# Kernel tuning notes

Measured on AMD Instinct MI355X. Metric: run time of the kernel, lower is better.

Reference implementation:

```python
import jax, jax.numpy as jnp
import numpy as np

B, F, E = 16384, 50, 64          # batch, field_size, embedding_size
V, D = 100000, 512               # feature_size, deep_init_size
H1, H2 = 1024, 512               # deep_layers
BN_EPS = 1e-10


def setup_inputs() -> dict:
    key = jax.random.key(0)
    ks = jax.random.split(key, 14)
    g0 = np.sqrt(6.0 / (D + H1))
    g1 = np.sqrt(6.0 / (H1 + H2))
    go = np.sqrt(5.0 / (D + 1))
    return {
        "feat_index": jax.random.randint(ks[0], (B, F), 0, V),
        "feat_value": jax.random.uniform(ks[1], (B, F), dtype=jnp.float32),
        "feature_embeddings": jax.random.normal(ks[2], (V, E), dtype=jnp.float32) * 0.01,
        "product_linear": jax.random.normal(ks[3], (D, F, E), dtype=jnp.float32) * 0.01,
        "product_bias": jax.random.normal(ks[4], (D,), dtype=jnp.float32),
        "product_quadratic_inner": jax.random.normal(ks[5], (D, F), dtype=jnp.float32) * 0.01,
        "layer_0": jax.random.uniform(ks[6], (D, H1), minval=-g0, maxval=g0, dtype=jnp.float32),
        "bias_0": jax.random.uniform(ks[7], (1, H1), minval=-g0, maxval=g0, dtype=jnp.float32),
        "layer_1": jax.random.uniform(ks[8], (H1, H2), minval=-g1, maxval=g1, dtype=jnp.float32),
        "bias_1": jax.random.uniform(ks[9], (1, H2), minval=-g1, maxval=g1, dtype=jnp.float32),
        "bn_scale": jax.random.normal(ks[10], (1,), dtype=jnp.float32) * 0.01,
        "bn_offset": jax.random.normal(ks[11], (1,), dtype=jnp.float32) * 0.01,
        "output_w": jax.random.uniform(ks[12], (H2, 1), minval=-go, maxval=go, dtype=jnp.float32),
        "output_b": jnp.float32(0.01),
    }


def reference(feat_index, feat_value, feature_embeddings, product_linear,
              product_bias, product_quadratic_inner, layer_0, bias_0,
              layer_1, bias_1, bn_scale, bn_offset, output_w, output_b):
    # embedding lookup scaled by feature values: (B, F, E)
    emb = feature_embeddings[feat_index] * feat_value[..., None]
    # linear product signal: sum over field+embed dims for each of D units
    lz = jnp.einsum('bfe,dfe->bd', emb, product_linear)          # (B, D)
    # inner quadratic signal: field-weighted sum then L2 norm over embed dim
    s = jnp.einsum('bfe,df->bde', emb, product_quadratic_inner)  # (B, D, E)
    lp = jnp.sqrt(jnp.sum(s * s, axis=-1))                       # (B, D)
    y = jax.nn.relu(lz + lp + product_bias)
    # dropout omitted (deterministic eval-mode reference)
    for W, bvec in ((layer_0, bias_0), (layer_1, bias_1)):
        y = y @ W + bvec
        m = jnp.mean(y, axis=0)
        v = jnp.var(y, axis=0)
        y = (y - m) * jax.lax.rsqrt(v + BN_EPS) * bn_scale + bn_offset
        y = jax.nn.relu(y)
    out = y @ output_w + output_b
    return jax.nn.sigmoid(out)
```

## Files before the change

### kernel.cpp

```cpp
#include <hip/hip_runtime.h>

typedef unsigned short u16;
typedef __attribute__((ext_vector_type(8))) short bf16x8v;
typedef __attribute__((ext_vector_type(4))) float f32x4v;

#define B_SZ 16384
#define F_SZ 50
#define E_SZ 64
#define D_SZ 512
#define H1_SZ 1024
#define H2_SZ 512
#define KP 4096

__device__ __forceinline__ float b2f(u16 u){
  union { unsigned int i; float f; } v; v.i = ((unsigned int)u) << 16; return v.f;
}
__device__ __forceinline__ u16 f2b(float f){
  union { float f; unsigned int i; } v; v.f = f;
  unsigned int r = v.i + 0x7FFFu + ((v.i >> 16) & 1u);
  return (u16)(r >> 16);
}

__device__ __forceinline__ void gload16(const u16* g, u16* lds_base_uniform){
#if __has_builtin(__builtin_amdgcn_global_load_lds)
  __builtin_amdgcn_global_load_lds(
      (const __attribute__((address_space(1))) unsigned int*)g,
      (__attribute__((address_space(3))) unsigned int*)lds_base_uniform,
      16, 0, 0);
#else
  int lane = threadIdx.x & 63;
  *(uint4*)(lds_base_uniform + lane*8) = *(const uint4*)g;
#endif
}

__device__ __forceinline__ void swz(int id, int nblog2, int &x, int &y){
  int xcd = id & 7, j = id >> 3;
  x = j & ((1 << nblog2) - 1);
  y = ((j >> nblog2) << 3) | xcd;
}

__global__ __launch_bounds__(256) void k_gather(
    const int* __restrict__ fidx, const float* __restrict__ fval,
    const float* __restrict__ femb, u16* __restrict__ embT)
{
  __shared__ int   sidx[F_SZ];
  __shared__ float sfv[F_SZ];
  __shared__ u16   tile[F_SZ*66];
  const int b = blockIdx.x, t = threadIdx.x;
  if (t < F_SZ){ sidx[t] = fidx[b*F_SZ+t]; sfv[t] = fval[b*F_SZ+t]; }
  __syncthreads();
  #pragma unroll
  for (int i=0;i<13;i++){
    int k = i*256+t;
    if (k < F_SZ*E_SZ){
      int f = k>>6, e = k&63;
      tile[f*66+e] = f2b(femb[(size_t)sidx[f]*E_SZ + e] * sfv[f]);
    }
  }
  __syncthreads();
  u16* orow = embT + (size_t)b*KP;
  #pragma unroll
  for (int i=0;i<16;i++){
    int k = i*256+t;
    int f = k&63, e = k>>6;
    orow[k] = (f < F_SZ) ? tile[f*66+e] : (u16)0;
  }
}

__global__ __launch_bounds__(256) void k_prep(
    const float* __restrict__ Wl, u16* __restrict__ WlT,
    const float* __restrict__ Pq, u16* __restrict__ PqTp,
    const float* __restrict__ w0, u16* __restrict__ w0T,
    const float* __restrict__ w1, u16* __restrict__ w1T,
    const float* __restrict__ pb, const float* __restrict__ b0,
    float* __restrict__ cvec)
{
  __shared__ u16 tile[F_SZ*66];
  const int r = blockIdx.x, t = threadIdx.x;
  if (r < 512){
    const int d = r;
    #pragma unroll
    for (int i=0;i<13;i++){
      int k = i*256+t;
      if (k < F_SZ*E_SZ) tile[(k>>6)*66 + (k&63)] = f2b(Wl[(size_t)d*(F_SZ*E_SZ) + k]);
    }
    __syncthreads();
    u16* orow = WlT + (size_t)d*KP;
    #pragma unroll
    for (int i=0;i<16;i++){
      int k = i*256+t;
      int f = k&63, e = k>>6;
      orow[k] = (f < F_SZ) ? tile[f*66+e] : (u16)0;
    }
  } else if (r < 640){
    int idx = (r-512)*256 + t;
    int d = idx >> 6, f = idx & 63;
    PqTp[idx] = (f < F_SZ) ? f2b(Pq[d*F_SZ + f]) : (u16)0;
  } else if (r < 2688){
    int idx = (r-640)*256 + t;
    int k = idx & 511, n = idx >> 9;
    w0T[idx] = f2b(w0[(size_t)k*H1_SZ + n]);
  } else if (r < 4736){
    int idx = (r-2688)*256 + t;
    int k = idx & 1023, n = idx >> 10;
    w1T[idx] = f2b(w1[(size_t)k*H2_SZ + n]);
  } else {
    int rr = r - 4736;
    int h = (rr & 3)*256 + t;
    int d0 = (rr >> 2)*64;
    float acc = (d0 == 0) ? b0[h] : 0.f;
    #pragma unroll 8
    for (int d=0; d<64; d++) acc += pb[d0+d]*w0[(size_t)(d0+d)*H1_SZ + h];
    atomicAdd(&cvec[h], acc);
  }
}


__global__ __launch_bounds__(256) void k_prod(
    const u16* __restrict__ A,
    const u16* __restrict__ Bm,
    const u16* __restrict__ Pp,
    const float* __restrict__ pbias,
    u16* __restrict__ y0)
{
  __shared__ __align__(16) u16 As[64*128];
  __shared__ __align__(16) u16 Bs[128*128];
  const int tid  = threadIdx.x;
  const int wave = tid >> 6, lane = tid & 63;
  const int quad = lane >> 4, l16 = lane & 15;
  int bx, by;  swz(blockIdx.x, 2, bx, by);
  const int n0 = bx * 128, m0 = by * 64;
  const int wr = wave >> 1, wc = wave & 1;
  const int lr4 = lane >> 4;
  const int cb  = lane & 15;
  const int sw  = (l16 & 7);

  bf16x8v pfr[4][2];
  #pragma unroll
  for (int nt=0;nt<4;nt++)
    #pragma unroll
    for (int ks=0;ks<2;ks++)
      pfr[nt][ks] = *(const bf16x8v*)&Pp[(n0 + wc*64 + nt*16 + l16)*64 + ks*32 + quad*8];

  f32x4v acc[2][4];
  f32x4v lpa[2][4];
  #pragma unroll
  for (int i=0;i<2;i++)
    #pragma unroll
    for (int j=0;j<4;j++){
      acc[i][j] = (f32x4v){0.f,0.f,0.f,0.f};
      lpa[i][j] = (f32x4v){0.f,0.f,0.f,0.f};
    }
  const f32x4v zz = {0.f,0.f,0.f,0.f};

  for (int k0 = 0; k0 < KP; k0 += 128){
    __syncthreads();
    #pragma unroll
    for (int c=0;c<4;c++){
      const int r0 = wave*16 + c*4;
      const int row = r0 + lr4;
      gload16(A + (size_t)(m0 + row)*KP + k0 + ((cb ^ (row & 7)) << 3), As + r0*128);
    }
    #pragma unroll
    for (int c=0;c<8;c++){
      const int r0 = wave*32 + c*4;
      const int row = r0 + lr4;
      gload16(Bm + (size_t)(n0 + row)*KP + k0 + ((cb ^ (row & 7)) << 3), Bs + r0*128);
    }
    __syncthreads();

    bf16x8v af[4][2];
    #pragma unroll
    for (int ks=0;ks<4;ks++)
      #pragma unroll
      for (int mt=0;mt<2;mt++)
        af[ks][mt] = *(const bf16x8v*)&As[(wr*32+mt*16+l16)*128 + (((ks*4+quad) ^ sw))*8];

    #pragma unroll
    for (int ks=0; ks<4; ks++){
      bf16x8v bfr[4];
      #pragma unroll
      for (int nt=0;nt<4;nt++)
        bfr[nt] = *(const bf16x8v*)&Bs[(wc*64+nt*16+l16)*128 + (((ks*4+quad) ^ sw))*8];
      #pragma unroll
      for (int mt=0;mt<2;mt++)
        #pragma unroll
        for (int nt=0;nt<4;nt++)
          acc[mt][nt] = __builtin_amdgcn_mfma_f32_16x16x32_bf16(af[ks][mt], bfr[nt], acc[mt][nt], 0, 0, 0);
    }

    #pragma unroll
    for (int h=0; h<2; h++){
      #pragma unroll
      for (int nt=0;nt<4;nt++){
        f32x4v s[2];
        #pragma unroll
        for (int mt=0;mt<2;mt++)
          s[mt] = __builtin_amdgcn_mfma_f32_16x16x32_bf16(af[2*h][mt],   pfr[nt][0], zz,    0, 0, 0);
        #pragma unroll
        for (int mt=0;mt<2;mt++)
          s[mt] = __builtin_amdgcn_mfma_f32_16x16x32_bf16(af[2*h+1][mt], pfr[nt][1], s[mt], 0, 0, 0);
        #pragma unroll
        for (int mt=0;mt<2;mt++)
          #pragma unroll
          for (int r=0;r<4;r++)
            lpa[mt][nt][r] = fmaf(s[mt][r], s[mt][r], lpa[mt][nt][r]);
      }
    }
  }

  #pragma unroll
  for (int nt=0;nt<4;nt++){
    const int n = n0 + wc*64 + nt*16 + l16;
    const float bv = pbias[n];
    #pragma unroll
    for (int mt=0;mt<2;mt++){
      const int mb = m0 + wr*32 + mt*16 + quad*4;
      #pragma unroll
      for (int r=0;r<4;r++){
        float v = acc[mt][nt][r] + sqrtf(lpa[mt][nt][r]) + bv;
        v = (v > 0.f ? v : 0.f) - bv;
        y0[(size_t)(mb+r)*D_SZ + n] = f2b(v);
      }
    }
  }
}

template<int DO_STATS, int CENTER, typename CT>
__global__ __launch_bounds__(256) void gemm_bt(
    const u16* __restrict__ A, const u16* __restrict__ Bm,
    CT* __restrict__ C, const float* __restrict__ bias,
    float* __restrict__ S1, float* __restrict__ S2,
    int nblog2, int N, int K)
{
  __shared__ __align__(16) u16 As[64*128];
  __shared__ __align__(16) u16 Bs[128*128];
  const int tid  = threadIdx.x;
  const int wave = tid >> 6, lane = tid & 63;
  const int quad = lane >> 4, l16 = lane & 15;
  int bx, by;  swz(blockIdx.x, nblog2, bx, by);
  const int n0 = bx * 128, m0 = by * 64;
  const int wr = wave >> 1, wc = wave & 1;
  const int lr4 = lane >> 4;
  const int cb  = lane & 15;
  const int sw  = (l16 & 7);

  f32x4v acc[2][4];
  #pragma unroll
  for (int i=0;i<2;i++)
    #pragma unroll
    for (int j=0;j<4;j++)
      acc[i][j] = (f32x4v){0.f,0.f,0.f,0.f};

  for (int k0 = 0; k0 < K; k0 += 128){
    __syncthreads();
    #pragma unroll
    for (int c=0;c<4;c++){
      const int r0 = wave*16 + c*4;
      const int row = r0 + lr4;
      gload16(A + (size_t)(m0 + row)*K + k0 + ((cb ^ (row & 7)) << 3), As + r0*128);
    }
    #pragma unroll
    for (int c=0;c<8;c++){
      const int r0 = wave*32 + c*4;
      const int row = r0 + lr4;
      gload16(Bm + (size_t)(n0 + row)*K + k0 + ((cb ^ (row & 7)) << 3), Bs + r0*128);
    }
    __syncthreads();
    #pragma unroll
    for (int ks=0; ks<4; ks++){
      bf16x8v af[2], bfr[4];
      #pragma unroll
      for (int mt=0;mt<2;mt++)
        af[mt] = *(const bf16x8v*)&As[(wr*32+mt*16+l16)*128 + (((ks*4+quad) ^ sw))*8];
      #pragma unroll
      for (int nt=0;nt<4;nt++)
        bfr[nt] = *(const bf16x8v*)&Bs[(wc*64+nt*16+l16)*128 + (((ks*4+quad) ^ sw))*8];
      #pragma unroll
      for (int mt=0;mt<2;mt++)
        #pragma unroll
        for (int nt=0;nt<4;nt++)
          acc[mt][nt] = __builtin_amdgcn_mfma_f32_16x16x32_bf16(af[mt], bfr[nt], acc[mt][nt], 0, 0, 0);
    }
  }

  #pragma unroll
  for (int nt=0;nt<4;nt++){
    const int n = n0 + wc*64 + nt*16 + l16;
    float bv = 0.f;
    if (DO_STATS) bv = bias[n];
    float ls1 = 0.f, ls2 = 0.f;
    #pragma unroll
    for (int mt=0;mt<2;mt++){
      const int mb = m0 + wr*32 + mt*16 + quad*4;
      #pragma unroll
      for (int r=0;r<4;r++){
        float v = acc[mt][nt][r] + bv;
        if constexpr (sizeof(CT) == 2) C[(size_t)(mb+r)*N + n] = f2b(CENTER ? acc[mt][nt][r] : v);
        else                           C[(size_t)(mb+r)*N + n] = v;
        ls1 += v; ls2 += v*v;
      }
    }
    if (DO_STATS){
      ls1 += __shfl_xor(ls1, 16); ls2 += __shfl_xor(ls2, 16);
      ls1 += __shfl_xor(ls1, 32); ls2 += __shfl_xor(ls2, 32);
      if (quad == 0){ atomicAdd(&S1[n], ls1); atomicAdd(&S2[n], ls2); }
    }
  }
}

__global__ void k_bnfin(const float* __restrict__ S1, const float* __restrict__ S2, int n,
                        const float* __restrict__ bnsc, const float* __restrict__ bnof,
                        const float* __restrict__ cadd,
                        float* __restrict__ Aout, float* __restrict__ Bout)
{
  int i = blockIdx.x*256 + threadIdx.x;
  if (i < n){
    const float invB = 1.f / 16384.f;
    float m   = S1[i]*invB;
    float var = S2[i]*invB - m*m;
    float a   = bnsc[0] * rsqrtf(var + 1e-10f);
    Aout[i] = a;
    Bout[i] = bnof[0] - m*a + a*cadd[i];
  }
}

__global__ __launch_bounds__(256) void k_bnapply(
    const u16* __restrict__ Z, u16* __restrict__ Y,
    const float* __restrict__ Aa, const float* __restrict__ Bb, int nmask)
{
  size_t base = ((size_t)blockIdx.x*256 + threadIdx.x) * 8;
  int n0 = (int)(base & (size_t)nmask);
  union { uint4 q; u16 s[8]; } z, o;
  z.q = *(const uint4*)&Z[base];
  #pragma unroll
  for (int j=0;j<8;j++){
    float v = b2f(z.s[j]) * Aa[n0+j] + Bb[n0+j];
    o.s[j] = f2b(v > 0.f ? v : 0.f);
  }
  *(uint4*)&Y[base] = o.q;
}

__global__ __launch_bounds__(256) void k_out(
    const u16* __restrict__ Z2, const float* __restrict__ wvec,
    const float* __restrict__ obp,
    const float* __restrict__ Aa, const float* __restrict__ Bb,
    float* __restrict__ out)
{
  const int wave = threadIdx.x >> 6, lane = threadIdx.x & 63;
  const int b = blockIdx.x*4 + wave;
  const int n0 = lane*8;
  union { uint4 q; u16 s[8]; } z;
  z.q = *(const uint4*)&Z2[(size_t)b*H2_SZ + n0];
  float4 wa = *(const float4*)&wvec[n0];
  float4 wb = *(const float4*)&wvec[n0+4];
  float wv[8] = {wa.x,wa.y,wa.z,wa.w,wb.x,wb.y,wb.z,wb.w};
  float s = 0.f;
  #pragma unroll
  for (int j=0;j<8;j++){
    float y = b2f(z.s[j]) * Aa[n0+j] + Bb[n0+j];
    y = y > 0.f ? y : 0.f;
    s += y * wv[j];
  }
  s += __shfl_xor(s,1);  s += __shfl_xor(s,2);  s += __shfl_xor(s,4);
  s += __shfl_xor(s,8);  s += __shfl_xor(s,16); s += __shfl_xor(s,32);
  if (lane == 0){
    float x = s + obp[0];
    out[b] = 1.f / (1.f + expf(-x));
  }
}


extern "C" void kernel_launch(void* const* d_in, const int* in_sizes, int n_in,
                              void* d_out, int out_size, void* d_ws, size_t ws_size,
                              hipStream_t stream)
{
  const int*   fidx  = (const int*)d_in[0];
  const float* fval  = (const float*)d_in[1];
  const float* femb  = (const float*)d_in[2];
  const float* wl    = (const float*)d_in[3];
  const float* pbias = (const float*)d_in[4];
  const float* pq    = (const float*)d_in[5];
  const float* w0    = (const float*)d_in[6];
  const float* b0    = (const float*)d_in[7];
  const float* w1    = (const float*)d_in[8];
  const float* b1    = (const float*)d_in[9];
  const float* bnsc  = (const float*)d_in[10];
  const float* bnof  = (const float*)d_in[11];
  const float* ow    = (const float*)d_in[12];
  const float* ob    = (const float*)d_in[13];
  float* out = (float*)d_out;

  char* ws = (char*)d_ws;
  u16*   embT = (u16*)(ws + 0);
  u16*   z1b  = (u16*)(ws + 0);
  u16*   y1b  = (u16*)(ws + 67108864);
  u16*   z2b  = (u16*)(ws + 100663296);
  u16*   wlT  = (u16*)(ws + 134217728);
  u16*   y0b  = (u16*)(ws + 138412032);
  u16*   w0T  = (u16*)(ws + 155189248);
  u16*   w1T  = (u16*)(ws + 156237824);
  float* S1a  = (float*)(ws + 174063616);
  float* S2a  = S1a + 1024;
  float* S1b  = S2a + 1024;
  float* S2b  = S1b + 512;
  float* cvec = S2b + 512;
  float* A0   = cvec + 1024;
  float* B0   = A0 + 1024;
  float* A1   = B0 + 1024;
  float* B1   = A1 + 512;
  u16*   pqT  = (u16*)(ws + 174096384);

  hipMemsetAsync((void*)S1a, 0, 16384, stream);

  k_gather<<<B_SZ, 256, 0, stream>>>(fidx, fval, femb, embT);
  k_prep<<<4768, 256, 0, stream>>>(wl, wlT, pq, pqT, w0, w0T, w1, w1T,
                                   pbias, b0, cvec);

  k_prod<<<1024, 256, 0, stream>>>(embT, wlT, pqT, pbias, y0b);

  gemm_bt<1,1,u16><<<2048, 256, 0, stream>>>(y0b, w0T, z1b, cvec, S1a, S2a,
                                             3, H1_SZ, D_SZ);
  k_bnfin<<<4, 256, 0, stream>>>(S1a, S2a, 1024, bnsc, bnof, cvec, A0, B0);
  k_bnapply<<<8192, 256, 0, stream>>>(z1b, y1b, A0, B0, 1023);

  gemm_bt<1,1,u16><<<1024, 256, 0, stream>>>(y1b, w1T, z2b, b1, S1b, S2b,
                                             2, H2_SZ, H1_SZ);
  k_bnfin<<<2, 256, 0, stream>>>(S1b, S2b, 512, bnsc, bnof, b1, A1, B1);

  k_out<<<4096, 256, 0, stream>>>(z2b, ow, ob, A1, B1, out);
}
```

Before: 387.6 us.

## Compute quadratic term via per-sample Gram matrix and packed upper-triangle GEMM

Rewrites the inner-product quadratic signal as a dot product between each sample's field Gram matrix (upper triangle, 1275 entries) and precomputed pairwise products of Pq weights. This replaces the per-tile MFMA-and-square path in k_prod with a second plain GEMM over K=1280. It also drops the padding of the linear-term K from 4096 to the natural 3200. The gather kernel now computes the Gram matrix with MFMAs and uses vectorized loads and stores. The trade-off is that the quadratic result now comes from the bf16-rounded Gram and Pq products, which may be less accurate, and fmaxf clamps cancellation error before the sqrt.

```diff
diff --git a/kernel.cpp b/kernel.cpp
--- a/kernel.cpp
+++ b/kernel.cpp
@@ -10,7 +10,8 @@
 #define D_SZ 512
 #define H1_SZ 1024
 #define H2_SZ 512
-#define KP 4096
+#define KL 3200
+#define KG 1280
 
 __device__ __forceinline__ float b2f(u16 u){
   union { unsigned int i; float f; } v; v.i = ((unsigned int)u) << 16; return v.f;
@@ -41,71 +42,104 @@
 
 __global__ __launch_bounds__(256) void k_gather(
     const int* __restrict__ fidx, const float* __restrict__ fval,
-    const float* __restrict__ femb, u16* __restrict__ embT)
+    const float* __restrict__ femb, u16* __restrict__ embT,
+    u16* __restrict__ Gp)
 {
   __shared__ int   sidx[F_SZ];
   __shared__ float sfv[F_SZ];
-  __shared__ u16   tile[F_SZ*66];
+  __shared__ __align__(16) u16 tile[64*72];
   const int b = blockIdx.x, t = threadIdx.x;
+  const int wave = t >> 6, lane = t & 63, quad = lane >> 4, l16 = lane & 15;
   if (t < F_SZ){ sidx[t] = fidx[b*F_SZ+t]; sfv[t] = fval[b*F_SZ+t]; }
   __syncthreads();
   #pragma unroll
-  for (int i=0;i<13;i++){
-    int k = i*256+t;
-    if (k < F_SZ*E_SZ){
-      int f = k>>6, e = k&63;
-      tile[f*66+e] = f2b(femb[(size_t)sidx[f]*E_SZ + e] * sfv[f]);
+  for (int i=0;i<4;i++){
+    int k4 = (i*256+t)*4;
+    if (k4 < F_SZ*E_SZ){
+      int f = k4>>6, e = k4&63;
+      float4 v = *(const float4*)&femb[(size_t)sidx[f]*E_SZ + e];
+      float s = sfv[f];
+      tile[f*72+e+0] = f2b(v.x*s);
+      tile[f*72+e+1] = f2b(v.y*s);
+      tile[f*72+e+2] = f2b(v.z*s);
+      tile[f*72+e+3] = f2b(v.w*s);
     }
   }
   __syncthreads();
-  u16* orow = embT + (size_t)b*KP;
-  #pragma unroll
-  for (int i=0;i<16;i++){
-    int k = i*256+t;
-    int f = k&63, e = k>>6;
-    orow[k] = (f < F_SZ) ? tile[f*66+e] : (u16)0;
-  }
+  u16* orow = embT + (size_t)b*KL;
+  #pragma unroll
+  for (int i=0;i<2;i++){
+    int k8 = (i*256+t)*8;
+    if (k8 < F_SZ*E_SZ){
+      int f = k8>>6, e0 = k8&63;
+      *(uint4*)&orow[k8] = *(const uint4*)&tile[f*72+e0];
+    }
+  }
+  u16* grow = Gp + (size_t)b*KG;
+  static const int TM[10] = {0,0,0,0,1,1,1,2,2,3};
+  static const int TN[10] = {0,1,2,3,1,2,3,2,3,3};
+  for (int ti = wave; ti < 10; ti += 4){
+    const int tm = TM[ti], tn = TN[ti];
+    f32x4v g = {0.f,0.f,0.f,0.f};
+    #pragma unroll
+    for (int ks=0;ks<2;ks++){
+      bf16x8v af = *(const bf16x8v*)&tile[(tm*16+l16)*72 + (ks*4+quad)*8];
+      bf16x8v bf = *(const bf16x8v*)&tile[(tn*16+l16)*72 + (ks*4+quad)*8];
+      g = __builtin_amdgcn_mfma_f32_16x16x32_bf16(af, bf, g, 0, 0, 0);
+    }
+    const int gn = tn*16 + l16;
+    #pragma unroll
+    for (int r=0;r<4;r++){
+      const int gm = tm*16 + quad*4 + r;
+      if (gm < F_SZ && gn < F_SZ && gn >= gm)
+        grow[gm*F_SZ - ((gm*(gm-1))>>1) + (gn-gm)] = f2b(g[r]);
+    }
+  }
+  if (t < 5) grow[1275+t] = 0;
 }
 
 __global__ __launch_bounds__(256) void k_prep(
     const float* __restrict__ Wl, u16* __restrict__ WlT,
-    const float* __restrict__ Pq, u16* __restrict__ PqTp,
+    const float* __restrict__ Pq, u16* __restrict__ pqq,
     const float* __restrict__ w0, u16* __restrict__ w0T,
     const float* __restrict__ w1, u16* __restrict__ w1T,
     const float* __restrict__ pb, const float* __restrict__ b0,
     float* __restrict__ cvec)
 {
-  __shared__ u16 tile[F_SZ*66];
   const int r = blockIdx.x, t = threadIdx.x;
   if (r < 512){
     const int d = r;
     #pragma unroll
-    for (int i=0;i<13;i++){
-      int k = i*256+t;
-      if (k < F_SZ*E_SZ) tile[(k>>6)*66 + (k&63)] = f2b(Wl[(size_t)d*(F_SZ*E_SZ) + k]);
-    }
-    __syncthreads();
-    u16* orow = WlT + (size_t)d*KP;
-    #pragma unroll
-    for (int i=0;i<16;i++){
-      int k = i*256+t;
-      int f = k&63, e = k>>6;
-      orow[k] = (f < F_SZ) ? tile[f*66+e] : (u16)0;
-    }
-  } else if (r < 640){
-    int idx = (r-512)*256 + t;
-    int d = idx >> 6, f = idx & 63;
-    PqTp[idx] = (f < F_SZ) ? f2b(Pq[d*F_SZ + f]) : (u16)0;
-  } else if (r < 2688){
-    int idx = (r-640)*256 + t;
+    for (int i=0;i<4;i++){
+      int k4 = (i*256+t)*4;
+      if (k4 < KL){
+        float4 v = *(const float4*)&Wl[(size_t)d*KL + k4];
+        u16* o = &WlT[(size_t)d*KL + k4];
+        o[0]=f2b(v.x); o[1]=f2b(v.y); o[2]=f2b(v.z); o[3]=f2b(v.w);
+      }
+    }
+  } else if (r < 1024){
+    const int d = r - 512;
+    const float* prow = &Pq[d*F_SZ];
+    u16* orow = &pqq[(size_t)d*KG];
+    int trif = 0;
+    for (int f=0; f<F_SZ; f++){
+      int len = F_SZ - f;
+      if (t < len)
+        orow[trif + t] = f2b(prow[f]*prow[f+t]*(t ? 2.f : 1.f));
+      trif += len;
+    }
+    if (t < 5) orow[1275+t] = 0;
+  } else if (r < 3072){
+    int idx = (r-1024)*256 + t;
     int k = idx & 511, n = idx >> 9;
     w0T[idx] = f2b(w0[(size_t)k*H1_SZ + n]);
-  } else if (r < 4736){
-    int idx = (r-2688)*256 + t;
+  } else if (r < 5120){
+    int idx = (r-3072)*256 + t;
     int k = idx & 1023, n = idx >> 10;
     w1T[idx] = f2b(w1[(size_t)k*H2_SZ + n]);
   } else {
-    int rr = r - 4736;
+    int rr = r - 5120;
     int h = (rr & 3)*256 + t;
     int d0 = (rr >> 2)*64;
     float acc = (d0 == 0) ? b0[h] : 0.f;
@@ -117,9 +151,10 @@
 
 
 __global__ __launch_bounds__(256) void k_prod(
-    const u16* __restrict__ A,
-    const u16* __restrict__ Bm,
-    const u16* __restrict__ Pp,
+    const u16* __restrict__ Ae,
+    const u16* __restrict__ Bw,
+    const u16* __restrict__ Ag,
+    const u16* __restrict__ Bq,
     const float* __restrict__ pbias,
     u16* __restrict__ y0)
 {
@@ -135,79 +170,51 @@
   const int cb  = lane & 15;
   const int sw  = (l16 & 7);
 
-  bf16x8v pfr[4][2];
-  #pragma unroll
-  for (int nt=0;nt<4;nt++)
-    #pragma unroll
-    for (int ks=0;ks<2;ks++)
-      pfr[nt][ks] = *(const bf16x8v*)&Pp[(n0 + wc*64 + nt*16 + l16)*64 + ks*32 + quad*8];
-
-  f32x4v acc[2][4];
-  f32x4v lpa[2][4];
+  f32x4v acc1[2][4], acc2[2][4];
   #pragma unroll
   for (int i=0;i<2;i++)
     #pragma unroll
     for (int j=0;j<4;j++){
-      acc[i][j] = (f32x4v){0.f,0.f,0.f,0.f};
-      lpa[i][j] = (f32x4v){0.f,0.f,0.f,0.f};
-    }
-  const f32x4v zz = {0.f,0.f,0.f,0.f};
-
-  for (int k0 = 0; k0 < KP; k0 += 128){
-    __syncthreads();
-    #pragma unroll
-    for (int c=0;c<4;c++){
-      const int r0 = wave*16 + c*4;
-      const int row = r0 + lr4;
-      gload16(A + (size_t)(m0 + row)*KP + k0 + ((cb ^ (row & 7)) << 3), As + r0*128);
-    }
-    #pragma unroll
-    for (int c=0;c<8;c++){
-      const int r0 = wave*32 + c*4;
-      const int row = r0 + lr4;
-      gload16(Bm + (size_t)(n0 + row)*KP + k0 + ((cb ^ (row & 7)) << 3), Bs + r0*128);
-    }
-    __syncthreads();
-
-    bf16x8v af[4][2];
-    #pragma unroll
-    for (int ks=0;ks<4;ks++)
-      #pragma unroll
-      for (int mt=0;mt<2;mt++)
-        af[ks][mt] = *(const bf16x8v*)&As[(wr*32+mt*16+l16)*128 + (((ks*4+quad) ^ sw))*8];
-
-    #pragma unroll
-    for (int ks=0; ks<4; ks++){
-      bf16x8v bfr[4];
-      #pragma unroll
-      for (int nt=0;nt<4;nt++)
-        bfr[nt] = *(const bf16x8v*)&Bs[(wc*64+nt*16+l16)*128 + (((ks*4+quad) ^ sw))*8];
-      #pragma unroll
-      for (int mt=0;mt<2;mt++)
+      acc1[i][j] = (f32x4v){0.f,0.f,0.f,0.f};
+      acc2[i][j] = (f32x4v){0.f,0.f,0.f,0.f};
+    }
+
+  auto run = [&](const u16* Ap, const u16* Bp, int K, f32x4v (&acc)[2][4]){
+    for (int k0 = 0; k0 < K; k0 += 128){
+      __syncthreads();
+      #pragma unroll
+      for (int c=0;c<4;c++){
+        const int r0 = wave*16 + c*4;
+        const int row = r0 + lr4;
+        gload16(Ap + (size_t)(m0 + row)*K + k0 + ((cb ^ (row & 7)) << 3), As + r0*128);
+      }
+      #pragma unroll
+      for (int c=0;c<8;c++){
+        const int r0 = wave*32 + c*4;
+        const int row = r0 + lr4;
+        gload16(Bp + (size_t)(n0 + row)*K + k0 + ((cb ^ (row & 7)) << 3), Bs + r0*128);
+      }
+      __syncthreads();
+      #pragma unroll
+      for (int ks=0; ks<4; ks++){
+        bf16x8v af[2], bfr[4];
+        #pragma unroll
+        for (int mt=0;mt<2;mt++)
+          af[mt] = *(const bf16x8v*)&As[(wr*32+mt*16+l16)*128 + (((ks*4+quad) ^ sw))*8];
         #pragma unroll
         for (int nt=0;nt<4;nt++)
-          acc[mt][nt] = __builtin_amdgcn_mfma_f32_16x16x32_bf16(af[ks][mt], bfr[nt], acc[mt][nt], 0, 0, 0);
-    }
-
-    #pragma unroll
-    for (int h=0; h<2; h++){
-      #pragma unroll
-      for (int nt=0;nt<4;nt++){
-        f32x4v s[2];
-        #pragma unroll
-        for (int mt=0;mt<2;mt++)
-          s[mt] = __builtin_amdgcn_mfma_f32_16x16x32_bf16(af[2*h][mt],   pfr[nt][0], zz,    0, 0, 0);
-        #pragma unroll
-        for (int mt=0;mt<2;mt++)
-          s[mt] = __builtin_amdgcn_mfma_f32_16x16x32_bf16(af[2*h+1][mt], pfr[nt][1], s[mt], 0, 0, 0);
+          bfr[nt] = *(const bf16x8v*)&Bs[(wc*64+nt*16+l16)*128 + (((ks*4+quad) ^ sw))*8];
         #pragma unroll
         for (int mt=0;mt<2;mt++)
           #pragma unroll
-          for (int r=0;r<4;r++)
-            lpa[mt][nt][r] = fmaf(s[mt][r], s[mt][r], lpa[mt][nt][r]);
-      }
-    }
-  }
+          for (int nt=0;nt<4;nt++)
+            acc[mt][nt] = __builtin_amdgcn_mfma_f32_16x16x32_bf16(af[mt], bfr[nt], acc[mt][nt], 0, 0, 0);
+      }
+    }
+  };
+
+  run(Ae, Bw, KL, acc1);
+  run(Ag, Bq, KG, acc2);
 
   #pragma unroll
   for (int nt=0;nt<4;nt++){
@@ -218,7 +225,7 @@
       const int mb = m0 + wr*32 + mt*16 + quad*4;
       #pragma unroll
       for (int r=0;r<4;r++){
-        float v = acc[mt][nt][r] + sqrtf(lpa[mt][nt][r]) + bv;
+        float v = acc1[mt][nt][r] + sqrtf(fmaxf(acc2[mt][nt][r], 0.f)) + bv;
         v = (v > 0.f ? v : 0.f) - bv;
         y0[(size_t)(mb+r)*D_SZ + n] = f2b(v);
       }
@@ -396,11 +403,13 @@
   u16*   z1b  = (u16*)(ws + 0);
   u16*   y1b  = (u16*)(ws + 67108864);
   u16*   z2b  = (u16*)(ws + 100663296);
-  u16*   wlT  = (u16*)(ws + 134217728);
-  u16*   y0b  = (u16*)(ws + 138412032);
-  u16*   w0T  = (u16*)(ws + 155189248);
-  u16*   w1T  = (u16*)(ws + 156237824);
-  float* S1a  = (float*)(ws + 174063616);
+  u16*   gpb  = (u16*)(ws + 104857600);
+  u16*   wlT  = (u16*)(ws + 146800640);
+  u16*   pqqb = (u16*)(ws + 150077440);
+  u16*   y0b  = (u16*)(ws + 151388160);
+  u16*   w0T  = (u16*)(ws + 168165376);
+  u16*   w1T  = (u16*)(ws + 169213952);
+  float* S1a  = (float*)(ws + 170262528);
   float* S2a  = S1a + 1024;
   float* S1b  = S2a + 1024;
   float* S2b  = S1b + 512;
@@ -409,15 +418,14 @@
   float* B0   = A0 + 1024;
   float* A1   = B0 + 1024;
   float* B1   = A1 + 512;
-  u16*   pqT  = (u16*)(ws + 174096384);
 
   hipMemsetAsync((void*)S1a, 0, 16384, stream);
 
-  k_gather<<<B_SZ, 256, 0, stream>>>(fidx, fval, femb, embT);
-  k_prep<<<4768, 256, 0, stream>>>(wl, wlT, pq, pqT, w0, w0T, w1, w1T,
+  k_gather<<<B_SZ, 256, 0, stream>>>(fidx, fval, femb, embT, gpb);
+  k_prep<<<5152, 256, 0, stream>>>(wl, wlT, pq, pqqb, w0, w0T, w1, w1T,
                                    pbias, b0, cvec);
 
-  k_prod<<<1024, 256, 0, stream>>>(embT, wlT, pqT, pbias, y0b);
+  k_prod<<<1024, 256, 0, stream>>>(embT, wlT, gpb, pqqb, pbias, y0b);
 
   gemm_bt<1,1,u16><<<2048, 256, 0, stream>>>(y0b, w0T, z1b, cvec, S1a, S2a,
                                              3, H1_SZ, D_SZ);
```

After: 362.2 us. 6.6% less time.
